# Kernel tuning notes

Measured on AMD Instinct MI355X. Metric: run time of the kernel, lower is better.

Reference implementation:

```python
import jax, jax.numpy as jnp
import numpy as np

B, L, S, V, I, H = 4096, 16, 512, 512, 512, 512  # batch, attn_length, attn_size, attn_vec_size, input_size, lstm hidden


def setup_inputs() -> dict:
    key = jax.random.key(0)
    ks = jax.random.split(key, 16)
    rn = lambda k, sh, sc=1.0: jax.random.normal(k, sh, dtype=jnp.float32) * sc
    return {
        "inputs": rn(ks[0], (B, I)),
        "cell_c": rn(ks[1], (B, H)),
        "cell_h": rn(ks[2], (B, H)),
        "attns": rn(ks[3], (B, S)),
        "attn_states": rn(ks[4], (B, L, S)),
        "W1": rn(ks[5], (I + S, I), 0.02),
        "b1": jnp.zeros((I,), jnp.float32),
        "Wx": rn(ks[6], (I, 4 * H), 0.02),
        "Wh": rn(ks[7], (H, 4 * H), 0.02),
        "b_lstm": jnp.zeros((4 * H,), jnp.float32),
        "W3": rn(ks[8], (2 * H, V), 0.02),
        "b3": jnp.zeros((V,), jnp.float32),
        "k": rn(ks[9], (1, 1, S, V), 0.02),
        "v": rn(ks[10], (1, 1, S, V), 0.02),
        "W2": rn(ks[11], (H + S, S), 0.02),
        "b2": jnp.zeros((S,), jnp.float32),
    }


def reference(inputs, cell_c, cell_h, attns, attn_states, W1, b1, Wx, Wh, b_lstm, W3, b3, k, v, W2, b2):
    # linear1: project [inputs; attns] -> cell input
    x = jnp.concatenate([inputs, attns], axis=1) @ W1 + b1  # [B, I]
    # LSTM cell step (gate order i, f, g, o)
    gates = x @ Wx + cell_h @ Wh + b_lstm  # [B, 4H]
    i, f, g, o = jnp.split(gates, 4, axis=1)
    c_new = jax.nn.sigmoid(f) * cell_c + jax.nn.sigmoid(i) * jnp.tanh(g)
    h_new = jax.nn.sigmoid(o) * jnp.tanh(c_new)
    # attention over attn_states with query = concat(new_state)
    query = jnp.concatenate([c_new, h_new], axis=1)  # [B, 2H]
    # 1x1 conv over [B, L, 1, S] with kernel [1,1,S,V] == matmul over S
    hf = jnp.einsum('bls,sv->blv', attn_states, k[0, 0])  # [B, L, V]
    y = query @ W3 + b3  # [B, V]
    t = jnp.tanh(hf + y[:, None, :])  # [B, L, V]
    # reduce_sum(v * t, [2,3]) with v [1,1,S,V] broadcast against t [B,L,1,V]
    # == einsum over V with v summed over its S axis (t independent of S axis)
    vsum = v[0, 0].sum(axis=0)  # [V]
    s = jnp.einsum('blv,v->bl', t, vsum)  # [B, L]
    a = jax.nn.softmax(s, axis=1)
    d = jnp.einsum('bl,bls->bs', a, attn_states)  # new_attns [B, S]
    # output projection on [cell_output; new_attns]
    output = jnp.concatenate([h_new, d], axis=1) @ W2 + b2  # [B, S]
    # shift attention window: drop oldest, append output
    new_attn_states = jnp.concatenate([attn_states[:, 1:, :], output[:, None, :]], axis=1)
    new_attn_states = new_attn_states.reshape(inputs.shape[0], L * S)
    return output, c_new, h_new, d, new_attn_states
```

## Files before the change

### kernel.cpp

```cpp
#include <hip/hip_runtime.h>
#include <hip/hip_bf16.h>
#include <math.h>

#define BB 4096
#define LL 16
#define SS 512
#define VV 512
#define II 512
#define HH 512

typedef __attribute__((ext_vector_type(4))) float f32x4;
typedef __attribute__((ext_vector_type(8))) short short8;

#define GLOBAL_AS __attribute__((address_space(1)))
#define LDS_AS __attribute__((address_space(3)))

__device__ __forceinline__ unsigned short f2bf(float f) {
    union { float f; unsigned u; } c; c.f = f;
    unsigned u = c.u + 0x7FFFu + ((c.u >> 16) & 1u);
    return (unsigned short)(u >> 16);
}
__device__ __forceinline__ float bf2f(unsigned short u) {
    union { unsigned u; float f; } c; c.u = ((unsigned)u) << 16;
    return c.f;
}
__device__ __forceinline__ float fast_tanh(float x) {
    return 1.f - 2.f / (__expf(2.f * x) + 1.f);
}

template<int MODE, int NF>
__global__ __launch_bounds__(256) void gemm_mfma(
    const ushort* __restrict__ A, const ushort* __restrict__ Bt,
    const float* __restrict__ bias, void* __restrict__ C, float* __restrict__ C2,
    int ldc, int M, int N, int K) {
    constexpr int BN = NF * 32;
    __shared__ ushort Als[128 * 64];
    __shared__ ushort Bls[BN * 64];
    const int tid  = threadIdx.x;
    const int lane = tid & 63;
    const int w    = tid >> 6;
    const int wm   = w >> 1, wn = w & 1;
    const int brow = blockIdx.y * 128;
    const int bcol = blockIdx.x * BN;
    f32x4 acc[4][NF] = {};
    const int nkt = K >> 6;
    for (int kt = 0; kt < nkt; ++kt) {
        __syncthreads();
        #pragma unroll
        for (int i = 0; i < 4; ++i) {
            int c0 = i * 256 + w * 64;
            int c  = c0 + lane;
            int row = c >> 3, sl = c & 7;
            const ushort* gp = A + (size_t)(brow + row) * K + kt * 64 + ((sl ^ (row & 7)) * 8);
            __builtin_amdgcn_global_load_lds((const GLOBAL_AS void*)gp,
                                             (LDS_AS void*)(Als + c0 * 8), 16, 0, 0);
        }
        #pragma unroll
        for (int i = 0; i < NF; ++i) {
            int c0 = i * 256 + w * 64;
            int c  = c0 + lane;
            int row = c >> 3, sl = c & 7;
            const ushort* gp = Bt + (size_t)(bcol + row) * K + kt * 64 + ((sl ^ (row & 7)) * 8);
            __builtin_amdgcn_global_load_lds((const GLOBAL_AS void*)gp,
                                             (LDS_AS void*)(Bls + c0 * 8), 16, 0, 0);
        }
        __syncthreads();
        const char* AlsB = (const char*)Als;
        const char* BlsB = (const char*)Bls;
        #pragma unroll
        for (int kh = 0; kh < 2; ++kh) {
            int ks = kh * 4 + (lane >> 4);
            short8 a[4], b[NF];
            #pragma unroll
            for (int m = 0; m < 4; ++m) {
                int row = wm * 64 + m * 16 + (lane & 15);
                a[m] = *(const short8*)(AlsB + (row * 8 + (ks ^ (row & 7))) * 16);
            }
            #pragma unroll
            for (int n = 0; n < NF; ++n) {
                int row = wn * (NF * 16) + n * 16 + (lane & 15);
                b[n] = *(const short8*)(BlsB + (row * 8 + (ks ^ (row & 7))) * 16);
            }
            #pragma unroll
            for (int m = 0; m < 4; ++m)
                #pragma unroll
                for (int n = 0; n < NF; ++n)
                    acc[m][n] = __builtin_amdgcn_mfma_f32_16x16x32_bf16(a[m], b[n], acc[m][n], 0, 0, 0);
        }
    }
    #pragma unroll
    for (int m = 0; m < 4; ++m)
        #pragma unroll
        for (int n = 0; n < NF; ++n)
            #pragma unroll
            for (int r = 0; r < 4; ++r) {
                int gm = brow + wm * 64 + m * 16 + (lane >> 4) * 4 + r;
                int gc = bcol + wn * (NF * 16) + n * 16 + (lane & 15);
                float v = acc[m][n][r] + bias[gc];
                if (MODE == 1) ((ushort*)C)[(size_t)gm * ldc + gc] = f2bf(v);
                else           ((float*)C)[(size_t)gm * ldc + gc] = v;
                if (MODE == 2) C2[((size_t)gm * 16 + 15) * 512 + gc] = v;
            }
}

__global__ __launch_bounds__(256) void gemm_gates(
    const ushort* __restrict__ A, const ushort* __restrict__ Bt,
    const float* __restrict__ bias, const float* __restrict__ cc,
    float* __restrict__ o_c, float* __restrict__ o_h,
    ushort* __restrict__ A4, ushort* __restrict__ A7) {
    __shared__ ushort Als[128 * 64];
    __shared__ ushort Bls[64 * 64];
    const int tid = threadIdx.x, lane = tid & 63, w = tid >> 6;
    const int l15 = lane & 15, l4 = lane >> 4;
    const int brow = blockIdx.y * 128;
    const int xb = blockIdx.x;
    f32x4 acc[2][4] = {};
    for (int kt = 0; kt < 16; ++kt) {
        __syncthreads();
        #pragma unroll
        for (int i = 0; i < 4; ++i) {
            int c0 = i * 256 + w * 64, c = c0 + lane;
            int row = c >> 3, sl = c & 7;
            const ushort* gp = A + (size_t)(brow + row) * 1024 + kt * 64 + ((sl ^ (row & 7)) * 8);
            __builtin_amdgcn_global_load_lds((const GLOBAL_AS void*)gp,
                                             (LDS_AS void*)(Als + c0 * 8), 16, 0, 0);
        }
        #pragma unroll
        for (int i = 0; i < 2; ++i) {
            int c0 = i * 256 + w * 64, c = c0 + lane;
            int row = c >> 3, sl = c & 7;
            const ushort* gp = Bt + (size_t)(xb * 64 + row) * 1024 + kt * 64 + ((sl ^ (row & 7)) * 8);
            __builtin_amdgcn_global_load_lds((const GLOBAL_AS void*)gp,
                                             (LDS_AS void*)(Bls + c0 * 8), 16, 0, 0);
        }
        __syncthreads();
        const char* AlsB = (const char*)Als;
        const char* BlsB = (const char*)Bls;
        #pragma unroll
        for (int kh = 0; kh < 2; ++kh) {
            int ks = kh * 4 + l4;
            short8 a[2], b[4];
            #pragma unroll
            for (int m = 0; m < 2; ++m) {
                int row = w * 32 + m * 16 + l15;
                a[m] = *(const short8*)(AlsB + (row * 8 + (ks ^ (row & 7))) * 16);
            }
            #pragma unroll
            for (int n = 0; n < 4; ++n) {
                int row = n * 16 + l15;
                b[n] = *(const short8*)(BlsB + (row * 8 + (ks ^ (row & 7))) * 16);
            }
            #pragma unroll
            for (int m = 0; m < 2; ++m)
                #pragma unroll
                for (int n = 0; n < 4; ++n)
                    acc[m][n] = __builtin_amdgcn_mfma_f32_16x16x32_bf16(a[m], b[n], acc[m][n], 0, 0, 0);
        }
    }
    const int h = xb * 16 + l15;
    #pragma unroll
    for (int m = 0; m < 2; ++m)
        #pragma unroll
        for (int r = 0; r < 4; ++r) {
            int gm = brow + w * 32 + m * 16 + l4 * 4 + r;
            float gi = acc[m][0][r] + bias[h];
            float gf = acc[m][1][r] + bias[512 + h];
            float gg = acc[m][2][r] + bias[1024 + h];
            float go = acc[m][3][r] + bias[1536 + h];
            float si = 1.f / (1.f + __expf(-gi));
            float sf = 1.f / (1.f + __expf(-gf));
            float so = 1.f / (1.f + __expf(-go));
            float cv = sf * cc[(size_t)gm * 512 + h] + si * tanhf(gg);
            float hn = so * tanhf(cv);
            o_c[(size_t)gm * 512 + h] = cv;
            o_h[(size_t)gm * 512 + h] = hn;
            A4[(size_t)gm * 1024 + h] = f2bf(cv);
            A4[(size_t)gm * 1024 + 512 + h] = f2bf(hn);
            A7[(size_t)gm * 1024 + h] = f2bf(hn);
        }
}

__global__ __launch_bounds__(512, 4) void score_all(
    const float* __restrict__ ASf, const ushort* __restrict__ Bt,
    const float* __restrict__ Y, const float* __restrict__ vsum,
    float* __restrict__ o_ns, float* __restrict__ o_d, ushort* __restrict__ A7) {
    __shared__ ushort Als[64 * 40];
    __shared__ ushort Bls[8][2][2048];
    __shared__ float sred[8][64];
    __shared__ float s_lds[64];
    const int tid  = threadIdx.x;
    const int lane = tid & 63;
    const int w    = tid >> 6;
    const int l15  = lane & 15, l4 = lane >> 4;
    const int brow = blockIdx.x * 64;
    const int bg0  = brow >> 4;
    const int arow = tid >> 3, aq = tid & 7;
    const float* agp = ASf + (size_t)(brow + arow) * 512 + aq * 4;
    const char* AlsB = (const char*)Als;
    f32x4 acc[4][4] = {};

    #pragma unroll
    for (int i = 0; i < 4; ++i) {
        int cl = i * 64 + lane;
        int r = cl >> 2, sl = cl & 3;
        const ushort* gp = Bt + (size_t)(w * 64 + r) * 512 + ((sl ^ ((r >> 1) & 3)) * 8);
        __builtin_amdgcn_global_load_lds((const GLOBAL_AS void*)gp,
            (LDS_AS void*)(&Bls[w][0][i * 512] + lane * 8), 16, 0, 0);
    }
    float4 af = *(const float4*)agp;

    #pragma unroll
    for (int kt = 0; kt < 16; ++kt) {
        const int buf = kt & 1;
        asm volatile("s_waitcnt lgkmcnt(0)" ::: "memory");
        __builtin_amdgcn_s_barrier();
        {
            ushort4 u; u.x = f2bf(af.x); u.y = f2bf(af.y); u.z = f2bf(af.z); u.w = f2bf(af.w);
            *(ushort4*)((char*)Als + arow * 80 + aq * 8) = u;
        }
        if (kt < 15) {
            #pragma unroll
            for (int i = 0; i < 4; ++i) {
                int cl = i * 64 + lane;
                int r = cl >> 2, sl = cl & 3;
                const ushort* gp = Bt + (size_t)(w * 64 + r) * 512 + (kt + 1) * 32
                                   + ((sl ^ ((r >> 1) & 3)) * 8);
                __builtin_amdgcn_global_load_lds((const GLOBAL_AS void*)gp,
                    (LDS_AS void*)(&Bls[w][buf ^ 1][i * 512] + lane * 8), 16, 0, 0);
            }
            af = *(const float4*)(agp + (kt + 1) * 32);
        }
        asm volatile("s_waitcnt lgkmcnt(0)" ::: "memory");
        __builtin_amdgcn_s_barrier();
        if (kt < 15) asm volatile("s_waitcnt vmcnt(5)" ::: "memory");
        else         asm volatile("s_waitcnt vmcnt(0)" ::: "memory");
        short8 a[4], b[4];
        #pragma unroll
        for (int m = 0; m < 4; ++m) {
            int row = m * 16 + l15;
            a[m] = *(const short8*)(AlsB + row * 80 + l4 * 16);
        }
        #pragma unroll
        for (int n = 0; n < 4; ++n) {
            int r = n * 16 + l15;
            int sl = l4 ^ ((r >> 1) & 3);
            b[n] = *(const short8*)((const char*)&Bls[w][buf][0] + r * 64 + sl * 16);
        }
        #pragma unroll
        for (int m = 0; m < 4; ++m)
            #pragma unroll
            for (int n = 0; n < 4; ++n)
                acc[m][n] = __builtin_amdgcn_mfma_f32_16x16x32_bf16(a[m], b[n], acc[m][n], 0, 0, 0);
    }

    float part[4][4] = {};
    #pragma unroll
    for (int m = 0; m < 4; ++m) {
        int yb = bg0 + m;
        #pragma unroll
        for (int n = 0; n < 4; ++n) {
            int gc = w * 64 + n * 16 + l15;
            float yv = Y[(size_t)yb * 512 + gc];
            float vs = vsum[gc];
            #pragma unroll
            for (int r = 0; r < 4; ++r)
                part[m][r] += fast_tanh(acc[m][n][r] + yv) * vs;
        }
    }
    #pragma unroll
    for (int m = 0; m < 4; ++m)
        #pragma unroll
        for (int r = 0; r < 4; ++r) {
            float v = part[m][r];
            v += __shfl_xor(v, 1); v += __shfl_xor(v, 2);
            v += __shfl_xor(v, 4); v += __shfl_xor(v, 8);
            if (l15 == 0) sred[w][m * 16 + l4 * 4 + r] = v;
        }
    __syncthreads();
    if (tid < 64) {
        float v = 0.f;
        #pragma unroll
        for (int q = 0; q < 8; ++q) v += sred[q][tid];
        s_lds[tid] = v;
    }
    __syncthreads();

    {
        const int bat = w >> 1;
        const int bg  = bg0 + bat;
        const int c   = (w & 1) * 256 + lane * 4;
        float mx = -1e30f;
        #pragma unroll
        for (int l = 0; l < LL; ++l) mx = fmaxf(mx, s_lds[bat * 16 + l]);
        float wgt[LL]; float sum = 0.f;
        #pragma unroll
        for (int l = 0; l < LL; ++l) { wgt[l] = __expf(s_lds[bat * 16 + l] - mx); sum += wgt[l]; }
        const float inv = 1.f / sum;
        float d0 = 0.f, d1 = 0.f, d2 = 0.f, d3 = 0.f;
        #pragma unroll
        for (int l = 0; l < LL; ++l) {
            float4 v = *(const float4*)(ASf + ((size_t)bg * 16 + l) * 512 + c);
            if (l >= 1)
                *(float4*)(o_ns + ((size_t)bg * 16 + l - 1) * 512 + c) = v;
            d0 += wgt[l] * v.x; d1 += wgt[l] * v.y;
            d2 += wgt[l] * v.z; d3 += wgt[l] * v.w;
        }
        d0 *= inv; d1 *= inv; d2 *= inv; d3 *= inv;
        float4 dv; dv.x = d0; dv.y = d1; dv.z = d2; dv.w = d3;
        *(float4*)(o_d + (size_t)bg * 512 + c) = dv;
        ushort4 uv; uv.x = f2bf(d0); uv.y = f2bf(d1); uv.z = f2bf(d2); uv.w = f2bf(d3);
        *(ushort4*)(A7 + (size_t)bg * 1024 + 512 + c) = uv;
    }
}

struct TrJob { const float* srcA; const float* srcB; int K0; ushort* dst; int N; int K; int perm; };
struct TrJobs { TrJob j[5]; };

__global__ void tr_cvt_all(TrJobs jobs) {
    TrJob jb = jobs.j[blockIdx.z];
    int bn = blockIdx.x, bk = blockIdx.y;
    if (bn * 32 >= jb.N || bk * 32 >= jb.K) return;
    __shared__ float tile[32][33];
    int tx = threadIdx.x, ty = threadIdx.y;
    #pragma unroll
    for (int j = 0; j < 4; ++j) {
        int k = bk * 32 + ty + j * 8;
        const float* s = (k < jb.K0) ? (jb.srcA + (size_t)k * jb.N)
                                     : (jb.srcB + (size_t)(k - jb.K0) * jb.N);
        tile[ty + j * 8][tx] = s[bn * 32 + tx];
    }
    __syncthreads();
    #pragma unroll
    for (int j = 0; j < 4; ++j) {
        int n = bn * 32 + ty + j * 8;
        int nd = n;
        if (jb.perm) {
            int g = n >> 9, u = n & 511;
            nd = (u >> 4) * 64 + g * 16 + (u & 15);
        }
        jb.dst[(size_t)nd * jb.K + bk * 32 + tx] = f2bf(tile[tx][ty + j * 8]);
    }
}

struct CvJobs { const float* src[3]; ushort* dst[3]; };
__global__ void cvt_all(CvJobs jobs) {
    const float* src = jobs.src[blockIdx.y];
    ushort* dst = jobs.dst[blockIdx.y];
    int idx = blockIdx.x * 256 + threadIdx.x;
    int i4 = idx & 127, row = idx >> 7;
    float4 v = *(const float4*)(src + (size_t)row * 512 + i4 * 4);
    ushort4 o; o.x = f2bf(v.x); o.y = f2bf(v.y); o.z = f2bf(v.z); o.w = f2bf(v.w);
    *(ushort4*)(dst + (size_t)row * 1024 + i4 * 4) = o;
}

__global__ void vsum_k(const float* __restrict__ Vm, float* __restrict__ out) {
    __shared__ float red[8][32];
    int tc = threadIdx.x & 31, ts = threadIdx.x >> 5;
    int v = blockIdx.x * 32 + tc;
    float acc = 0.f;
    for (int s = ts; s < SS; s += 8) acc += Vm[(size_t)s * VV + v];
    red[ts][tc] = acc;
    __syncthreads();
    if (ts == 0) {
        float t = 0.f;
        #pragma unroll
        for (int j = 0; j < 8; ++j) t += red[j][tc];
        out[v] = t;
    }
}

extern "C" void kernel_launch(void* const* d_in, const int* in_sizes, int n_in,
                              void* d_out, int out_size, void* d_ws, size_t ws_size,
                              hipStream_t stream) {
    const float* inputs      = (const float*)d_in[0];
    const float* cell_c      = (const float*)d_in[1];
    const float* cell_h      = (const float*)d_in[2];
    const float* attns       = (const float*)d_in[3];
    const float* attn_states = (const float*)d_in[4];
    const float* W1          = (const float*)d_in[5];
    const float* b1          = (const float*)d_in[6];
    const float* Wx          = (const float*)d_in[7];
    const float* Wh          = (const float*)d_in[8];
    const float* b_lstm      = (const float*)d_in[9];
    const float* W3          = (const float*)d_in[10];
    const float* b3          = (const float*)d_in[11];
    const float* kmat        = (const float*)d_in[12];
    const float* vmat        = (const float*)d_in[13];
    const float* W2          = (const float*)d_in[14];
    const float* b2          = (const float*)d_in[15];

    float* o_out = (float*)d_out;
    float* o_c   = o_out + (size_t)BB * HH;
    float* o_h   = o_c   + (size_t)BB * HH;
    float* o_d   = o_h   + (size_t)BB * HH;
    float* o_ns  = o_d   + (size_t)BB * SS;

    float* ws_y     = (float*)d_ws;
    float* ws_vsum  = ws_y + (size_t)BB * VV;
    ushort* A1    = (ushort*)(ws_vsum + VV);
    ushort* A2    = A1 + (size_t)BB * 1024;
    ushort* A4    = A2 + (size_t)BB * 1024;
    ushort* A7    = A4 + (size_t)BB * 1024;
    ushort* W1t   = A7 + (size_t)BB * 1024;
    ushort* WBt   = W1t + (size_t)512 * 1024;
    ushort* W3t   = WBt + (size_t)2048 * 1024;
    ushort* W2t   = W3t + (size_t)512 * 1024;
    ushort* kTt   = W2t + (size_t)512 * 1024;

    TrJobs tj;
    tj.j[0] = {W1, W1, 1024, W1t, 512, 1024, 0};
    tj.j[1] = {Wx, Wh, 512, WBt, 2048, 1024, 1};
    tj.j[2] = {W3, W3, 1024, W3t, 512, 1024, 0};
    tj.j[3] = {W2, W2, 1024, W2t, 512, 1024, 0};
    tj.j[4] = {kmat, kmat, 512, kTt, 512, 512, 0};
    tr_cvt_all<<<dim3(64, 32, 5), dim3(32, 8), 0, stream>>>(tj);
    CvJobs cj;
    cj.src[0] = inputs; cj.dst[0] = A1;
    cj.src[1] = attns;  cj.dst[1] = A1 + 512;
    cj.src[2] = cell_h; cj.dst[2] = A2 + 512;
    cvt_all<<<dim3(BB * 128 / 256, 3), 256, 0, stream>>>(cj);
    vsum_k<<<16, 256, 0, stream>>>(vmat, ws_vsum);

    gemm_mfma<1, 1><<<dim3(512 / 32, BB / 128), 256, 0, stream>>>(
        A1, W1t, b1, A2, nullptr, 1024, BB, 512, 1024);
    gemm_gates<<<dim3(32, BB / 128), 256, 0, stream>>>(
        A2, WBt, b_lstm, cell_c, o_c, o_h, A4, A7);
    gemm_mfma<0, 1><<<dim3(512 / 32, BB / 128), 256, 0, stream>>>(
        A4, W3t, b3, ws_y, nullptr, 512, BB, 512, 1024);
    score_all<<<BB * LL / 64, 512, 0, stream>>>(
        attn_states, kTt, ws_y, ws_vsum, o_ns, o_d, A7);
    gemm_mfma<2, 1><<<dim3(512 / 32, BB / 128), 256, 0, stream>>>(
        A7, W2t, b2, o_out, o_ns, 512, BB, 512, 1024);
}
```

Before: 244.5 us.

## Fuse fp32-to-bf16 input conversion into linear1 GEMM and restructure score kernel tiling

Adds a gemm_x kernel that reads inputs and attns as fp32 directly and converts them to bf16 while staging into swizzled LDS. This removes the separate conversion pass and the A1 workspace round trip. score_all is reworked to use K-tiles of 64 with a single buffer holding the full 512-column B tile in LDS, XOR-swizzled layouts and s_setprio around the MFMA block. It drops the previous double-buffered, per-wave B pipeline, so load/compute overlap may be lost and the larger LDS footprint may lower occupancy.

```diff
diff --git a/kernel.cpp b/kernel.cpp
--- a/kernel.cpp
+++ b/kernel.cpp
@@ -103,6 +103,77 @@
             }
 }
 
+__global__ __launch_bounds__(256) void gemm_x(
+    const float* __restrict__ S0, const float* __restrict__ S1,
+    const ushort* __restrict__ Bt, const float* __restrict__ bias,
+    ushort* __restrict__ C, int ldc) {
+    __shared__ ushort Als[128 * 64];
+    __shared__ ushort Bls[32 * 64];
+    const int tid  = threadIdx.x;
+    const int lane = tid & 63;
+    const int w    = tid >> 6;
+    const int wm   = w >> 1, wn = w & 1;
+    const int brow = blockIdx.y * 128;
+    const int bcol = blockIdx.x * 32;
+    f32x4 acc[4][1] = {};
+    for (int kt = 0; kt < 16; ++kt) {
+        __syncthreads();
+        const float* src = (kt < 8) ? S0 : S1;
+        const int kbase = (kt & 7) * 64;
+        #pragma unroll
+        for (int i = 0; i < 4; ++i) {
+            int chunk = i * 256 + tid;
+            int row = chunk >> 3, slot = chunk & 7;
+            int gslot = slot ^ (row & 7);
+            const float* gp = src + (size_t)(brow + row) * 512 + kbase + gslot * 8;
+            float4 f0 = *(const float4*)gp;
+            float4 f1 = *(const float4*)(gp + 4);
+            short8 pk;
+            pk[0] = (short)f2bf(f0.x); pk[1] = (short)f2bf(f0.y);
+            pk[2] = (short)f2bf(f0.z); pk[3] = (short)f2bf(f0.w);
+            pk[4] = (short)f2bf(f1.x); pk[5] = (short)f2bf(f1.y);
+            pk[6] = (short)f2bf(f1.z); pk[7] = (short)f2bf(f1.w);
+            *(short8*)((char*)Als + chunk * 16) = pk;
+        }
+        {
+            int c0 = w * 64;
+            int c  = c0 + lane;
+            int row = c >> 3, sl = c & 7;
+            const ushort* gp = Bt + (size_t)(bcol + row) * 1024 + kt * 64 + ((sl ^ (row & 7)) * 8);
+            __builtin_amdgcn_global_load_lds((const GLOBAL_AS void*)gp,
+                                             (LDS_AS void*)(Bls + c0 * 8), 16, 0, 0);
+        }
+        __syncthreads();
+        const char* AlsB = (const char*)Als;
+        const char* BlsB = (const char*)Bls;
+        #pragma unroll
+        for (int kh = 0; kh < 2; ++kh) {
+            int ks = kh * 4 + (lane >> 4);
+            short8 a[4], b;
+            #pragma unroll
+            for (int m = 0; m < 4; ++m) {
+                int row = wm * 64 + m * 16 + (lane & 15);
+                a[m] = *(const short8*)(AlsB + (row * 8 + (ks ^ (row & 7))) * 16);
+            }
+            {
+                int row = wn * 16 + (lane & 15);
+                b = *(const short8*)(BlsB + (row * 8 + (ks ^ (row & 7))) * 16);
+            }
+            #pragma unroll
+            for (int m = 0; m < 4; ++m)
+                acc[m][0] = __builtin_amdgcn_mfma_f32_16x16x32_bf16(a[m], b, acc[m][0], 0, 0, 0);
+        }
+    }
+    #pragma unroll
+    for (int m = 0; m < 4; ++m)
+        #pragma unroll
+        for (int r = 0; r < 4; ++r) {
+            int gm = brow + wm * 64 + m * 16 + (lane >> 4) * 4 + r;
+            int gc = bcol + wn * 16 + (lane & 15);
+            C[(size_t)gm * ldc + gc] = f2bf(acc[m][0][r] + bias[gc]);
+        }
+}
+
 __global__ __launch_bounds__(256) void gemm_gates(
     const ushort* __restrict__ A, const ushort* __restrict__ Bt,
     const float* __restrict__ bias, const float* __restrict__ cc,
@@ -184,8 +255,8 @@
     const float* __restrict__ ASf, const ushort* __restrict__ Bt,
     const float* __restrict__ Y, const float* __restrict__ vsum,
     float* __restrict__ o_ns, float* __restrict__ o_d, ushort* __restrict__ A7) {
-    __shared__ ushort Als[64 * 40];
-    __shared__ ushort Bls[8][2][2048];
+    __shared__ ushort Als[64 * 64];
+    __shared__ ushort Bls[512 * 64];
     __shared__ float sred[8][64];
     __shared__ float s_lds[64];
     const int tid  = threadIdx.x;
@@ -194,65 +265,58 @@
     const int l15  = lane & 15, l4 = lane >> 4;
     const int brow = blockIdx.x * 64;
     const int bg0  = brow >> 4;
-    const int arow = tid >> 3, aq = tid & 7;
-    const float* agp = ASf + (size_t)(brow + arow) * 512 + aq * 4;
-    const char* AlsB = (const char*)Als;
     f32x4 acc[4][4] = {};
-
-    #pragma unroll
-    for (int i = 0; i < 4; ++i) {
-        int cl = i * 64 + lane;
-        int r = cl >> 2, sl = cl & 3;
-        const ushort* gp = Bt + (size_t)(w * 64 + r) * 512 + ((sl ^ ((r >> 1) & 3)) * 8);
-        __builtin_amdgcn_global_load_lds((const GLOBAL_AS void*)gp,
-            (LDS_AS void*)(&Bls[w][0][i * 512] + lane * 8), 16, 0, 0);
-    }
-    float4 af = *(const float4*)agp;
-
-    #pragma unroll
-    for (int kt = 0; kt < 16; ++kt) {
-        const int buf = kt & 1;
-        asm volatile("s_waitcnt lgkmcnt(0)" ::: "memory");
-        __builtin_amdgcn_s_barrier();
+    for (int kt = 0; kt < 8; ++kt) {
+        __syncthreads();
         {
-            ushort4 u; u.x = f2bf(af.x); u.y = f2bf(af.y); u.z = f2bf(af.z); u.w = f2bf(af.w);
-            *(ushort4*)((char*)Als + arow * 80 + aq * 8) = u;
-        }
-        if (kt < 15) {
-            #pragma unroll
-            for (int i = 0; i < 4; ++i) {
-                int cl = i * 64 + lane;
-                int r = cl >> 2, sl = cl & 3;
-                const ushort* gp = Bt + (size_t)(w * 64 + r) * 512 + (kt + 1) * 32
-                                   + ((sl ^ ((r >> 1) & 3)) * 8);
-                __builtin_amdgcn_global_load_lds((const GLOBAL_AS void*)gp,
-                    (LDS_AS void*)(&Bls[w][buf ^ 1][i * 512] + lane * 8), 16, 0, 0);
-            }
-            af = *(const float4*)(agp + (kt + 1) * 32);
-        }
-        asm volatile("s_waitcnt lgkmcnt(0)" ::: "memory");
-        __builtin_amdgcn_s_barrier();
-        if (kt < 15) asm volatile("s_waitcnt vmcnt(5)" ::: "memory");
-        else         asm volatile("s_waitcnt vmcnt(0)" ::: "memory");
-        short8 a[4], b[4];
-        #pragma unroll
-        for (int m = 0; m < 4; ++m) {
-            int row = m * 16 + l15;
-            a[m] = *(const short8*)(AlsB + row * 80 + l4 * 16);
-        }
-        #pragma unroll
-        for (int n = 0; n < 4; ++n) {
-            int r = n * 16 + l15;
-            int sl = l4 ^ ((r >> 1) & 3);
-            b[n] = *(const short8*)((const char*)&Bls[w][buf][0] + r * 64 + sl * 16);
-        }
-        #pragma unroll
-        for (int m = 0; m < 4; ++m)
-            #pragma unroll
-            for (int n = 0; n < 4; ++n)
-                acc[m][n] = __builtin_amdgcn_mfma_f32_16x16x32_bf16(a[m], b[n], acc[m][n], 0, 0, 0);
-    }
-
+            int chunk = tid;
+            int row = chunk >> 3, slot = chunk & 7;
+            int gslot = slot ^ (row & 7);
+            const float* gp = ASf + (size_t)(brow + row) * 512 + kt * 64 + gslot * 8;
+            float4 f0 = *(const float4*)gp;
+            float4 f1 = *(const float4*)(gp + 4);
+            short8 pk;
+            pk[0] = (short)f2bf(f0.x); pk[1] = (short)f2bf(f0.y);
+            pk[2] = (short)f2bf(f0.z); pk[3] = (short)f2bf(f0.w);
+            pk[4] = (short)f2bf(f1.x); pk[5] = (short)f2bf(f1.y);
+            pk[6] = (short)f2bf(f1.z); pk[7] = (short)f2bf(f1.w);
+            *(short8*)((char*)Als + chunk * 16) = pk;
+        }
+        #pragma unroll
+        for (int i = 0; i < 8; ++i) {
+            int c0 = i * 512 + w * 64;
+            int c  = c0 + lane;
+            int row = c >> 3, sl = c & 7;
+            const ushort* gp = Bt + (size_t)row * 512 + kt * 64 + ((sl ^ (row & 7)) * 8);
+            __builtin_amdgcn_global_load_lds((const GLOBAL_AS void*)gp,
+                                             (LDS_AS void*)(Bls + c0 * 8), 16, 0, 0);
+        }
+        __syncthreads();
+        const char* AlsB = (const char*)Als;
+        const char* BlsB = (const char*)Bls;
+        #pragma unroll
+        for (int kh = 0; kh < 2; ++kh) {
+            int ks = kh * 4 + l4;
+            short8 a[4], b[4];
+            #pragma unroll
+            for (int m = 0; m < 4; ++m) {
+                int row = m * 16 + l15;
+                a[m] = *(const short8*)(AlsB + (row * 8 + (ks ^ (row & 7))) * 16);
+            }
+            #pragma unroll
+            for (int n = 0; n < 4; ++n) {
+                int rowb = w * 64 + n * 16 + l15;
+                b[n] = *(const short8*)(BlsB + (rowb * 8 + (ks ^ (rowb & 7))) * 16);
+            }
+            __builtin_amdgcn_s_setprio(1);
+            #pragma unroll
+            for (int m = 0; m < 4; ++m)
+                #pragma unroll
+                for (int n = 0; n < 4; ++n)
+                    acc[m][n] = __builtin_amdgcn_mfma_f32_16x16x32_bf16(a[m], b[n], acc[m][n], 0, 0, 0);
+            __builtin_amdgcn_s_setprio(0);
+        }
+    }
     float part[4][4] = {};
     #pragma unroll
     for (int m = 0; m < 4; ++m) {
@@ -342,10 +406,7 @@
     }
 }
 
-struct CvJobs { const float* src[3]; ushort* dst[3]; };
-__global__ void cvt_all(CvJobs jobs) {
-    const float* src = jobs.src[blockIdx.y];
-    ushort* dst = jobs.dst[blockIdx.y];
+__global__ void cvt_ch(const float* __restrict__ src, ushort* __restrict__ dst) {
     int idx = blockIdx.x * 256 + threadIdx.x;
     int i4 = idx & 127, row = idx >> 7;
     float4 v = *(const float4*)(src + (size_t)row * 512 + i4 * 4);
@@ -397,8 +458,7 @@
 
     float* ws_y     = (float*)d_ws;
     float* ws_vsum  = ws_y + (size_t)BB * VV;
-    ushort* A1    = (ushort*)(ws_vsum + VV);
-    ushort* A2    = A1 + (size_t)BB * 1024;
+    ushort* A2    = (ushort*)(ws_vsum + VV);
     ushort* A4    = A2 + (size_t)BB * 1024;
     ushort* A7    = A4 + (size_t)BB * 1024;
     ushort* W1t   = A7 + (size_t)BB * 1024;
@@ -414,15 +474,11 @@
     tj.j[3] = {W2, W2, 1024, W2t, 512, 1024, 0};
     tj.j[4] = {kmat, kmat, 512, kTt, 512, 512, 0};
     tr_cvt_all<<<dim3(64, 32, 5), dim3(32, 8), 0, stream>>>(tj);
-    CvJobs cj;
-    cj.src[0] = inputs; cj.dst[0] = A1;
-    cj.src[1] = attns;  cj.dst[1] = A1 + 512;
-    cj.src[2] = cell_h; cj.dst[2] = A2 + 512;
-    cvt_all<<<dim3(BB * 128 / 256, 3), 256, 0, stream>>>(cj);
+    cvt_ch<<<BB * 128 / 256, 256, 0, stream>>>(cell_h, A2 + 512);
     vsum_k<<<16, 256, 0, stream>>>(vmat, ws_vsum);
 
-    gemm_mfma<1, 1><<<dim3(512 / 32, BB / 128), 256, 0, stream>>>(
-        A1, W1t, b1, A2, nullptr, 1024, BB, 512, 1024);
+    gemm_x<<<dim3(512 / 32, BB / 128), 256, 0, stream>>>(
+        inputs, attns, W1t, b1, A2, 1024);
     gemm_gates<<<dim3(32, BB / 128), 256, 0, stream>>>(
         A2, WBt, b_lstm, cell_c, o_c, o_h, A4, A7);
     gemm_mfma<0, 1><<<dim3(512 / 32, BB / 128), 256, 0, stream>>>(
```

Result: slower. 256.4 us (+4.9%).

## Replace double-buffered score_all K-loop with single-buffer 64-wide K tiles

Applied to the files above, without the earlier changes.

The score_all GEMM mainloop drops its per-wave double-buffered B staging (K-step 32, 16 iterations, manual vmcnt waits) for a single shared B tile of all 512 columns with K-step 64 over 8 iterations, synchronized by __syncthreads. A is now loaded as two float4s per thread, converted to bf16, and stored into an XOR-swizzled LDS tile. The aim is fewer barriers and iterations and bank-conflict-free LDS reads. In exchange, loads are no longer overlapped with MFMA work, and LDS use grows to about 72 KB per block, which may lower occupancy.

```diff
diff --git a/kernel.cpp b/kernel.cpp
--- a/kernel.cpp
+++ b/kernel.cpp
@@ -184,8 +184,8 @@
     const float* __restrict__ ASf, const ushort* __restrict__ Bt,
     const float* __restrict__ Y, const float* __restrict__ vsum,
     float* __restrict__ o_ns, float* __restrict__ o_d, ushort* __restrict__ A7) {
-    __shared__ ushort Als[64 * 40];
-    __shared__ ushort Bls[8][2][2048];
+    __shared__ ushort Als[64 * 64];
+    __shared__ ushort Bls[512 * 64];
     __shared__ float sred[8][64];
     __shared__ float s_lds[64];
     const int tid  = threadIdx.x;
@@ -194,65 +194,56 @@
     const int l15  = lane & 15, l4 = lane >> 4;
     const int brow = blockIdx.x * 64;
     const int bg0  = brow >> 4;
-    const int arow = tid >> 3, aq = tid & 7;
-    const float* agp = ASf + (size_t)(brow + arow) * 512 + aq * 4;
-    const char* AlsB = (const char*)Als;
     f32x4 acc[4][4] = {};
-
-    #pragma unroll
-    for (int i = 0; i < 4; ++i) {
-        int cl = i * 64 + lane;
-        int r = cl >> 2, sl = cl & 3;
-        const ushort* gp = Bt + (size_t)(w * 64 + r) * 512 + ((sl ^ ((r >> 1) & 3)) * 8);
-        __builtin_amdgcn_global_load_lds((const GLOBAL_AS void*)gp,
-            (LDS_AS void*)(&Bls[w][0][i * 512] + lane * 8), 16, 0, 0);
-    }
-    float4 af = *(const float4*)agp;
-
-    #pragma unroll
-    for (int kt = 0; kt < 16; ++kt) {
-        const int buf = kt & 1;
-        asm volatile("s_waitcnt lgkmcnt(0)" ::: "memory");
-        __builtin_amdgcn_s_barrier();
+    for (int kt = 0; kt < 8; ++kt) {
+        __syncthreads();
+        #pragma unroll
+        for (int i = 0; i < 8; ++i) {
+            int c0 = i * 512 + w * 64;
+            int c  = c0 + lane;
+            int row = c >> 3, sl = c & 7;
+            const ushort* gp = Bt + (size_t)row * 512 + kt * 64 + ((sl ^ (row & 7)) * 8);
+            __builtin_amdgcn_global_load_lds((const GLOBAL_AS void*)gp,
+                                             (LDS_AS void*)(Bls + c0 * 8), 16, 0, 0);
+        }
         {
-            ushort4 u; u.x = f2bf(af.x); u.y = f2bf(af.y); u.z = f2bf(af.z); u.w = f2bf(af.w);
-            *(ushort4*)((char*)Als + arow * 80 + aq * 8) = u;
-        }
-        if (kt < 15) {
-            #pragma unroll
-            for (int i = 0; i < 4; ++i) {
-                int cl = i * 64 + lane;
-                int r = cl >> 2, sl = cl & 3;
-                const ushort* gp = Bt + (size_t)(w * 64 + r) * 512 + (kt + 1) * 32
-                                   + ((sl ^ ((r >> 1) & 3)) * 8);
-                __builtin_amdgcn_global_load_lds((const GLOBAL_AS void*)gp,
-                    (LDS_AS void*)(&Bls[w][buf ^ 1][i * 512] + lane * 8), 16, 0, 0);
-            }
-            af = *(const float4*)(agp + (kt + 1) * 32);
-        }
-        asm volatile("s_waitcnt lgkmcnt(0)" ::: "memory");
-        __builtin_amdgcn_s_barrier();
-        if (kt < 15) asm volatile("s_waitcnt vmcnt(5)" ::: "memory");
-        else         asm volatile("s_waitcnt vmcnt(0)" ::: "memory");
-        short8 a[4], b[4];
-        #pragma unroll
-        for (int m = 0; m < 4; ++m) {
-            int row = m * 16 + l15;
-            a[m] = *(const short8*)(AlsB + row * 80 + l4 * 16);
-        }
-        #pragma unroll
-        for (int n = 0; n < 4; ++n) {
-            int r = n * 16 + l15;
-            int sl = l4 ^ ((r >> 1) & 3);
-            b[n] = *(const short8*)((const char*)&Bls[w][buf][0] + r * 64 + sl * 16);
-        }
-        #pragma unroll
-        for (int m = 0; m < 4; ++m)
-            #pragma unroll
-            for (int n = 0; n < 4; ++n)
-                acc[m][n] = __builtin_amdgcn_mfma_f32_16x16x32_bf16(a[m], b[n], acc[m][n], 0, 0, 0);
-    }
-
+            int chunk = tid;
+            int row = chunk >> 3, slot = chunk & 7;
+            int gslot = slot ^ (row & 7);
+            const float* gp = ASf + (size_t)(brow + row) * 512 + kt * 64 + gslot * 8;
+            float4 f0 = *(const float4*)gp;
+            float4 f1 = *(const float4*)(gp + 4);
+            short8 pk;
+            pk[0] = (short)f2bf(f0.x); pk[1] = (short)f2bf(f0.y);
+            pk[2] = (short)f2bf(f0.z); pk[3] = (short)f2bf(f0.w);
+            pk[4] = (short)f2bf(f1.x); pk[5] = (short)f2bf(f1.y);
+            pk[6] = (short)f2bf(f1.z); pk[7] = (short)f2bf(f1.w);
+            *(short8*)((char*)Als + chunk * 16) = pk;
+        }
+        __syncthreads();
+        const char* AlsB = (const char*)Als;
+        const char* BlsB = (const char*)Bls;
+        #pragma unroll
+        for (int kh = 0; kh < 2; ++kh) {
+            int ks = kh * 4 + l4;
+            short8 a[4], b[4];
+            #pragma unroll
+            for (int m = 0; m < 4; ++m) {
+                int row = m * 16 + l15;
+                a[m] = *(const short8*)(AlsB + (row * 8 + (ks ^ (row & 7))) * 16);
+            }
+            #pragma unroll
+            for (int n = 0; n < 4; ++n) {
+                int rowb = w * 64 + n * 16 + l15;
+                b[n] = *(const short8*)(BlsB + (rowb * 8 + (ks ^ (rowb & 7))) * 16);
+            }
+            #pragma unroll
+            for (int m = 0; m < 4; ++m)
+                #pragma unroll
+                for (int n = 0; n < 4; ++n)
+                    acc[m][n] = __builtin_amdgcn_mfma_f32_16x16x32_bf16(a[m], b[n], acc[m][n], 0, 0, 0);
+        }
+    }
     float part[4][4] = {};
     #pragma unroll
     for (int m = 0; m < 4; ++m) {
```

After: 226.8 us. -7.2%, faster.
